# Kernel tuning notes

Measured on AMD Instinct MI355X. Metric: run time of the kernel, lower is better.

## Reference

```python
import jax, jax.numpy as jnp
import numpy as np

DIM = 1024

def setup_inputs() -> dict:
    key = jax.random.key(0)
    ks = jax.random.split(key, 7)
    s = 1.0 / np.sqrt(DIM)  # roughly match nn.Linear init scale
    return {
        "x": jax.random.normal(ks[0], (4, 2048, DIM), dtype=jnp.float32),
        "Wq": jax.random.normal(ks[1], (DIM, DIM), dtype=jnp.float32) * s,
        "bq": jax.random.normal(ks[2], (DIM,), dtype=jnp.float32) * s,
        "Wk": jax.random.normal(ks[3], (DIM, DIM), dtype=jnp.float32) * s,
        "bk": jax.random.normal(ks[4], (DIM,), dtype=jnp.float32) * s,
        "Wv": jax.random.normal(ks[5], (DIM, DIM), dtype=jnp.float32) * s,
        "bv": jax.random.normal(ks[6], (DIM,), dtype=jnp.float32) * s,
    }

def reference(x, Wq, bq, Wk, bk, Wv, bv):
    # torch Linear: y = x @ W.T + b
    C = x.shape[-1]
    scale = C ** (-0.5)
    q = jnp.einsum('bnc,dc->bnd', x, Wq) + bq
    k = jnp.einsum('bnc,dc->bnd', x, Wk) + bk
    v = jnp.einsum('bnc,dc->bnd', x, Wv) + bv
    attn = jnp.einsum('bnd,bmd->bnm', q, k) * scale  # [B,N,N]
    attn = jax.nn.softmax(attn, axis=-1)
    out = jnp.einsum('bnm,bmd->bnd', attn, v)
    return out
```

## Files before the change

kernel.cpp:

```cpp
#include <hip/hip_runtime.h>

#define SEQ  2048
#define DIM  1024
#define NTOK 8192
#define NQKV 3072

typedef __attribute__((ext_vector_type(8))) __bf16 bf16x8;
typedef __attribute__((ext_vector_type(4))) float  f32x4;

__device__ __forceinline__ unsigned short f2bf(float f) {
    unsigned int u = __float_as_uint(f);
    u += 0x7fffu + ((u >> 16) & 1u);
    return (unsigned short)(u >> 16);
}

__device__ __forceinline__ float bfu2f(unsigned int lo16) {
    return __uint_as_float(lo16 << 16);
}

__device__ __forceinline__ void load_lds_128(const unsigned short* g, unsigned short* l) {
    __builtin_amdgcn_global_load_lds(
        (const __attribute__((address_space(1))) void*)g,
        (__attribute__((address_space(3))) void*)l, 16, 0, 0);
}

#define BAR() asm volatile("s_barrier" ::: "memory")

template <int MODE, int MB>
__global__ __launch_bounds__(512, 2)
void gemm2(const unsigned short* __restrict__ A, const unsigned short* __restrict__ B,
           void* __restrict__ Cv,
           const float* __restrict__ b0v, const float* __restrict__ b1v,
           const float* __restrict__ b2v, unsigned short* __restrict__ vt,
           const float* __restrict__ inv_rs,
           int K, int lda, int ldb, int ldc,
           long sA, long sB, long sC, float alpha)
{
    constexpr int BM = MB * 128;
    constexpr int AT = BM * 64;
    constexpr int BT = 256 * 64;
    constexpr int MH = MB * 2;
    __shared__ __align__(16) unsigned short As[2 * AT];
    __shared__ __align__(16) unsigned short Bs[2 * BT];

    const int tid  = threadIdx.x;
    const int wave = tid >> 6;
    const int lane = tid & 63;
    const int l4   = lane & 15;
    const int lh   = lane >> 4;
    const int wm   = wave >> 2;
    const int wn   = wave & 3;

    const int m0 = blockIdx.x * BM;
    const int n0 = blockIdx.y * 256;
    const int z  = blockIdx.z;
    A += (long)z * sA;
    B += (long)z * sB;

    const int r0 = tid >> 3;
    const int gc = (tid & 7) ^ (r0 & 7);
    const unsigned short* Ag = A + (long)(m0 + r0) * lda + gc * 8;
    const unsigned short* Bg = B + (long)(n0 + r0) * ldb + gc * 8;
    unsigned short* Al = As + tid * 8;
    unsigned short* Bl = Bs + tid * 8;

    const int NT = K >> 6;

    auto stage = [&](int t, int u) {
        const long kof = (long)t * 64;
#pragma unroll
        for (int p = 0; p < 2 * MB; ++p)
            load_lds_128(Ag + kof + (long)(64 * p) * lda, Al + u * AT + p * 4096);
#pragma unroll
        for (int p = 0; p < 4; ++p)
            load_lds_128(Bg + kof + (long)(64 * p) * ldb, Bl + u * BT + p * 4096);
    };

    const int aoff = (wm * (BM / 2) + l4) * 64;
    const int boff = (wn * 64 + l4) * 64;
    const int cs0  = ((0 + lh) ^ (lane & 7)) * 8;
    const int cs1  = ((4 + lh) ^ (lane & 7)) * 8;

    f32x4 acc[4 * MB][4] = {};
    bf16x8 alo[MH][2], ahi[MH][2], bfr[4][2];

    stage(0, 0);
    asm volatile("s_waitcnt vmcnt(0)" ::: "memory");
    BAR();

    for (int t = 0; t < NT; ++t) {
        const int u = t & 1;
        const unsigned short* Ab = As + u * AT + aoff;
        const unsigned short* Bb = Bs + u * BT + boff;

        if (t + 1 < NT) stage(t + 1, u ^ 1);

#pragma unroll
        for (int nf = 0; nf < 4; ++nf) {
            bfr[nf][0] = *(const bf16x8*)(Bb + nf * 1024 + cs0);
            bfr[nf][1] = *(const bf16x8*)(Bb + nf * 1024 + cs1);
        }
#pragma unroll
        for (int mf = 0; mf < MH; ++mf) {
            alo[mf][0] = *(const bf16x8*)(Ab + mf * 1024 + cs0);
            alo[mf][1] = *(const bf16x8*)(Ab + mf * 1024 + cs1);
        }
#pragma unroll
        for (int mf = 0; mf < MH; ++mf) {
            ahi[mf][0] = *(const bf16x8*)(Ab + (MH + mf) * 1024 + cs0);
            ahi[mf][1] = *(const bf16x8*)(Ab + (MH + mf) * 1024 + cs1);
        }

        __builtin_amdgcn_s_setprio(1);
#pragma unroll
        for (int mf = 0; mf < MH; ++mf)
#pragma unroll
            for (int nf = 0; nf < 2; ++nf)
#pragma unroll
                for (int kk = 0; kk < 2; ++kk)
                    acc[mf][nf] = __builtin_amdgcn_mfma_f32_16x16x32_bf16(
                        alo[mf][kk], bfr[nf][kk], acc[mf][nf], 0, 0, 0);
        __builtin_amdgcn_s_setprio(0);
        __builtin_amdgcn_s_setprio(1);
#pragma unroll
        for (int mf = 0; mf < MH; ++mf)
#pragma unroll
            for (int nf = 2; nf < 4; ++nf)
#pragma unroll
                for (int kk = 0; kk < 2; ++kk)
                    acc[mf][nf] = __builtin_amdgcn_mfma_f32_16x16x32_bf16(
                        alo[mf][kk], bfr[nf][kk], acc[mf][nf], 0, 0, 0);
        __builtin_amdgcn_s_setprio(0);
        __builtin_amdgcn_s_setprio(1);
#pragma unroll
        for (int mf = 0; mf < MH; ++mf)
#pragma unroll
            for (int nf = 2; nf < 4; ++nf)
#pragma unroll
                for (int kk = 0; kk < 2; ++kk)
                    acc[MH + mf][nf] = __builtin_amdgcn_mfma_f32_16x16x32_bf16(
                        ahi[mf][kk], bfr[nf][kk], acc[MH + mf][nf], 0, 0, 0);
        __builtin_amdgcn_s_setprio(0);
        __builtin_amdgcn_s_setprio(1);
#pragma unroll
        for (int mf = 0; mf < MH; ++mf)
#pragma unroll
            for (int nf = 0; nf < 2; ++nf)
#pragma unroll
                for (int kk = 0; kk < 2; ++kk)
                    acc[MH + mf][nf] = __builtin_amdgcn_mfma_f32_16x16x32_bf16(
                        ahi[mf][kk], bfr[nf][kk], acc[MH + mf][nf], 0, 0, 0);
        __builtin_amdgcn_s_setprio(0);

        asm volatile("s_waitcnt vmcnt(0) lgkmcnt(0)" ::: "memory");
        BAR();
    }

    const int r0c = m0 + wm * (BM / 2) + lh * 4;
    const int c0c = n0 + wn * 64 + l4;

    if (MODE == 0) {
        if (n0 >= 2048) {
#pragma unroll
            for (int nf = 0; nf < 4; ++nf) {
                const int d = c0c + nf * 16 - 2048;
                const float bias = b2v[d];
#pragma unroll
                for (int mf = 0; mf < 4 * MB; ++mf) {
                    const int row = r0c + mf * 16;
                    const int bb = row >> 11;
                    const int mm = row & 2047;
                    ushort4 u;
                    u.x = f2bf(acc[mf][nf][0] + bias);
                    u.y = f2bf(acc[mf][nf][1] + bias);
                    u.z = f2bf(acc[mf][nf][2] + bias);
                    u.w = f2bf(acc[mf][nf][3] + bias);
                    *(ushort4*)(vt + ((long)bb * DIM + d) * SEQ + mm) = u;
                }
            }
        } else {
            unsigned short* C16 = (unsigned short*)Cv;
#pragma unroll
            for (int nf = 0; nf < 4; ++nf) {
                const int col = c0c + nf * 16;
                const float bias = (col >= 1024) ? b1v[col - 1024] : b0v[col];
#pragma unroll
                for (int mf = 0; mf < 4 * MB; ++mf)
#pragma unroll
                    for (int r = 0; r < 4; ++r)
                        C16[(long)(r0c + mf * 16 + r) * ldc + col] =
                            f2bf(acc[mf][nf][r] + bias);
            }
        }
    } else if (MODE == 1) {
        float* C = (float*)Cv + (long)z * sC;
        const float* ir = inv_rs + (long)z * SEQ;
#pragma unroll
        for (int mf = 0; mf < 4 * MB; ++mf) {
            const int row = r0c + mf * 16;
            const float4 inv4 = *(const float4*)(ir + row);
#pragma unroll
            for (int nf = 0; nf < 4; ++nf) {
                const int col = c0c + nf * 16;
                C[(long)(row + 0) * ldc + col] = acc[mf][nf][0] * inv4.x;
                C[(long)(row + 1) * ldc + col] = acc[mf][nf][1] * inv4.y;
                C[(long)(row + 2) * ldc + col] = acc[mf][nf][2] * inv4.z;
                C[(long)(row + 3) * ldc + col] = acc[mf][nf][3] * inv4.w;
            }
        }
    } else {
        unsigned short* C16 = (unsigned short*)Cv + (long)z * sC;
#pragma unroll
        for (int nf = 0; nf < 4; ++nf) {
            const int col = c0c + nf * 16;
#pragma unroll
            for (int mf = 0; mf < 4 * MB; ++mf)
#pragma unroll
                for (int r = 0; r < 4; ++r)
                    C16[(long)(r0c + mf * 16 + r) * ldc + col] =
                        f2bf(__expf(acc[mf][nf][r] * alpha));
        }
    }
}

__global__ __launch_bounds__(256)
void cvt_x(const float* __restrict__ src, unsigned short* __restrict__ dst, int n4)
{
    int i = blockIdx.x * 256 + threadIdx.x;
    if (i < n4) {
        float4 f = ((const float4*)src)[i];
        ushort4 u;
        u.x = f2bf(f.x); u.y = f2bf(f.y); u.z = f2bf(f.z); u.w = f2bf(f.w);
        ((ushort4*)dst)[i] = u;
    }
}

__global__ __launch_bounds__(256)
void cvt_w3(const float* __restrict__ Wq, const float* __restrict__ Wk,
            const float* __restrict__ Wv, unsigned short* __restrict__ dst)
{
    const int sel = blockIdx.y;
    const float* src = (sel == 0) ? Wq : ((sel == 1) ? Wk : Wv);
    const int i = blockIdx.x * 256 + threadIdx.x;
    float4 f = ((const float4*)src)[i];
    ushort4 u;
    u.x = f2bf(f.x); u.y = f2bf(f.y); u.z = f2bf(f.z); u.w = f2bf(f.w);
    ((ushort4*)(dst + (long)sel * DIM * DIM))[i] = u;
}

__global__ __launch_bounds__(256)
void rowsum_inv(const unsigned short* __restrict__ P, float* __restrict__ inv_rs)
{
    const int row  = blockIdx.x * 4 + (threadIdx.x >> 6);
    const int lane = threadIdx.x & 63;
    const unsigned short* pr = P + (long)row * SEQ;

    float s = 0.f;
#pragma unroll
    for (int it = 0; it < 4; ++it) {
        uint4 u = *(const uint4*)(pr + (it * 64 + lane) * 8);
        s += bfu2f(u.x & 0xffffu) + __uint_as_float(u.x & 0xffff0000u);
        s += bfu2f(u.y & 0xffffu) + __uint_as_float(u.y & 0xffff0000u);
        s += bfu2f(u.z & 0xffffu) + __uint_as_float(u.z & 0xffff0000u);
        s += bfu2f(u.w & 0xffffu) + __uint_as_float(u.w & 0xffff0000u);
    }
    for (int off = 32; off > 0; off >>= 1)
        s += __shfl_xor(s, off);
    if (lane == 0) inv_rs[row] = 1.0f / s;
}

extern "C" void kernel_launch(void* const* d_in, const int* in_sizes, int n_in,
                              void* d_out, int out_size, void* d_ws, size_t ws_size,
                              hipStream_t stream)
{
    const float* x  = (const float*)d_in[0];
    const float* Wq = (const float*)d_in[1];
    const float* bq = (const float*)d_in[2];
    const float* Wk = (const float*)d_in[3];
    const float* bk = (const float*)d_in[4];
    const float* Wv = (const float*)d_in[5];
    const float* bv = (const float*)d_in[6];
    float* out = (float*)d_out;

    char* ws = (char*)d_ws;
    unsigned short* xb   = (unsigned short*)ws;
    unsigned short* Wb   = (unsigned short*)(ws + 16u * 1024 * 1024);
    unsigned short* qkv  = (unsigned short*)(ws + 64u * 1024 * 1024);
    unsigned short* vt   = (unsigned short*)(ws + 112u * 1024 * 1024);
    unsigned short* P    = (unsigned short*)(ws + 128u * 1024 * 1024);
    float*          irs  = (float*)(ws + 160u * 1024 * 1024);

    const float scale = 0.03125f;
    dim3 blk(256);
    dim3 blk512(512);

    cvt_x<<<NTOK * DIM / 4 / 256, blk, 0, stream>>>(x, xb, NTOK * DIM / 4);
    cvt_w3<<<dim3(DIM * DIM / 4 / 256, 3), blk, 0, stream>>>(Wq, Wk, Wv, Wb);

    gemm2<0, 2><<<dim3(NTOK / 256, NQKV / 256), blk512, 0, stream>>>(
        xb, Wb, qkv, bq, bk, bv, vt, nullptr,
        DIM, DIM, DIM, NQKV, 0, 0, 0, 1.0f);

    gemm2<2, 2><<<dim3(SEQ / 256, SEQ / 256, 4), blk512, 0, stream>>>(
        qkv, qkv + 1024, P, nullptr, nullptr, nullptr, nullptr, nullptr,
        DIM, NQKV, NQKV, SEQ,
        (long)SEQ * NQKV, (long)SEQ * NQKV, (long)SEQ * SEQ, scale);

    rowsum_inv<<<NTOK / 4, blk, 0, stream>>>(P, irs);

    gemm2<1, 1><<<dim3(SEQ / 128, DIM / 256, 4), blk512, 0, stream>>>(
        P, vt, out, nullptr, nullptr, nullptr, nullptr, irs,
        SEQ, SEQ, SEQ, DIM,
        (long)SEQ * SEQ, (long)DIM * SEQ, (long)SEQ * DIM, 1.0f);
}
```

Measured before the change: 272.9 us.

## Overlap next-tile prefetch and barrier with MFMA clusters, shrink QKV GEMM tile

Restructures the GEMM main loop. All fragments are now read from LDS before the next-tile global→LDS stage is issued. The ahi fragment loads are interleaved between MFMA clusters. The wait/barrier moves ahead of the last MFMA cluster so synchronisation overlaps with compute. The QKV projection GEMM also switches from 256-row to 128-row tiles (MB=1), doubling its grid, to improve occupancy and wave balance. The added risk is the reordered wait and barrier: the final cluster runs after the barrier using register fragments, which is only safe if every LDS read has completed first.

```diff
diff --git a/kernel.cpp b/kernel.cpp
--- a/kernel.cpp
+++ b/kernel.cpp
@@ -25,6 +25,22 @@
 }
 
 #define BAR() asm volatile("s_barrier" ::: "memory")
+
+#define CLUSTER(AFR, NB, MBASE)                                            \
+    do {                                                                   \
+        __builtin_amdgcn_s_setprio(1);                                     \
+        _Pragma("unroll")                                                  \
+        for (int mf = 0; mf < 4; ++mf)                                     \
+            _Pragma("unroll")                                              \
+            for (int nn = 0; nn < 2; ++nn)                                 \
+                _Pragma("unroll")                                          \
+                for (int kk = 0; kk < 2; ++kk)                             \
+                    acc[(MBASE) + mf][(NB) + nn] =                         \
+                        __builtin_amdgcn_mfma_f32_16x16x32_bf16(           \
+                            AFR[mf][kk], bfr[(NB) + nn][kk],               \
+                            acc[(MBASE) + mf][(NB) + nn], 0, 0, 0);        \
+        __builtin_amdgcn_s_setprio(0);                                     \
+    } while (0)
 
 template <int MODE, int MB>
 __global__ __launch_bounds__(512, 2)
@@ -39,7 +55,6 @@
     constexpr int BM = MB * 128;
     constexpr int AT = BM * 64;
     constexpr int BT = 256 * 64;
-    constexpr int MH = MB * 2;
     __shared__ __align__(16) unsigned short As[2 * AT];
     __shared__ __align__(16) unsigned short Bs[2 * BT];
 
@@ -82,7 +97,7 @@
     const int cs1  = ((4 + lh) ^ (lane & 7)) * 8;
 
     f32x4 acc[4 * MB][4] = {};
-    bf16x8 alo[MH][2], ahi[MH][2], bfr[4][2];
+    bf16x8 bfr[4][2], alo[4][2], ahi[4][2];
 
     stage(0, 0);
     asm volatile("s_waitcnt vmcnt(0)" ::: "memory");
@@ -93,67 +108,41 @@
         const unsigned short* Ab = As + u * AT + aoff;
         const unsigned short* Bb = Bs + u * BT + boff;
 
-        if (t + 1 < NT) stage(t + 1, u ^ 1);
-
-#pragma unroll
-        for (int nf = 0; nf < 4; ++nf) {
-            bfr[nf][0] = *(const bf16x8*)(Bb + nf * 1024 + cs0);
-            bfr[nf][1] = *(const bf16x8*)(Bb + nf * 1024 + cs1);
-        }
-#pragma unroll
-        for (int mf = 0; mf < MH; ++mf) {
+#pragma unroll
+        for (int nn = 0; nn < 2; ++nn) {
+            bfr[nn][0] = *(const bf16x8*)(Bb + nn * 1024 + cs0);
+            bfr[nn][1] = *(const bf16x8*)(Bb + nn * 1024 + cs1);
+        }
+#pragma unroll
+        for (int mf = 0; mf < 4; ++mf) {
             alo[mf][0] = *(const bf16x8*)(Ab + mf * 1024 + cs0);
             alo[mf][1] = *(const bf16x8*)(Ab + mf * 1024 + cs1);
         }
 #pragma unroll
-        for (int mf = 0; mf < MH; ++mf) {
-            ahi[mf][0] = *(const bf16x8*)(Ab + (MH + mf) * 1024 + cs0);
-            ahi[mf][1] = *(const bf16x8*)(Ab + (MH + mf) * 1024 + cs1);
-        }
-
-        __builtin_amdgcn_s_setprio(1);
-#pragma unroll
-        for (int mf = 0; mf < MH; ++mf)
-#pragma unroll
-            for (int nf = 0; nf < 2; ++nf)
-#pragma unroll
-                for (int kk = 0; kk < 2; ++kk)
-                    acc[mf][nf] = __builtin_amdgcn_mfma_f32_16x16x32_bf16(
-                        alo[mf][kk], bfr[nf][kk], acc[mf][nf], 0, 0, 0);
-        __builtin_amdgcn_s_setprio(0);
-        __builtin_amdgcn_s_setprio(1);
-#pragma unroll
-        for (int mf = 0; mf < MH; ++mf)
-#pragma unroll
-            for (int nf = 2; nf < 4; ++nf)
-#pragma unroll
-                for (int kk = 0; kk < 2; ++kk)
-                    acc[mf][nf] = __builtin_amdgcn_mfma_f32_16x16x32_bf16(
-                        alo[mf][kk], bfr[nf][kk], acc[mf][nf], 0, 0, 0);
-        __builtin_amdgcn_s_setprio(0);
-        __builtin_amdgcn_s_setprio(1);
-#pragma unroll
-        for (int mf = 0; mf < MH; ++mf)
-#pragma unroll
-            for (int nf = 2; nf < 4; ++nf)
-#pragma unroll
-                for (int kk = 0; kk < 2; ++kk)
-                    acc[MH + mf][nf] = __builtin_amdgcn_mfma_f32_16x16x32_bf16(
-                        ahi[mf][kk], bfr[nf][kk], acc[MH + mf][nf], 0, 0, 0);
-        __builtin_amdgcn_s_setprio(0);
-        __builtin_amdgcn_s_setprio(1);
-#pragma unroll
-        for (int mf = 0; mf < MH; ++mf)
-#pragma unroll
-            for (int nf = 0; nf < 2; ++nf)
-#pragma unroll
-                for (int kk = 0; kk < 2; ++kk)
-                    acc[MH + mf][nf] = __builtin_amdgcn_mfma_f32_16x16x32_bf16(
-                        ahi[mf][kk], bfr[nf][kk], acc[MH + mf][nf], 0, 0, 0);
-        __builtin_amdgcn_s_setprio(0);
-
-        asm volatile("s_waitcnt vmcnt(0) lgkmcnt(0)" ::: "memory");
-        BAR();
+        for (int nn = 2; nn < 4; ++nn) {
+            bfr[nn][0] = *(const bf16x8*)(Bb + nn * 1024 + cs0);
+            bfr[nn][1] = *(const bf16x8*)(Bb + nn * 1024 + cs1);
+        }
+        if (t + 1 < NT) stage(t + 1, u ^ 1);
+
+        if constexpr (MB == 2) {
+            CLUSTER(alo, 0, 0);
+#pragma unroll
+            for (int mf = 0; mf < 4; ++mf) {
+                ahi[mf][0] = *(const bf16x8*)(Ab + (4 + mf) * 1024 + cs0);
+                ahi[mf][1] = *(const bf16x8*)(Ab + (4 + mf) * 1024 + cs1);
+            }
+            CLUSTER(alo, 2, 0);
+            CLUSTER(ahi, 2, 4);
+            asm volatile("s_waitcnt vmcnt(0) lgkmcnt(0)" ::: "memory");
+            BAR();
+            CLUSTER(ahi, 0, 4);
+        } else {
+            CLUSTER(alo, 0, 0);
+            asm volatile("s_waitcnt vmcnt(0) lgkmcnt(0)" ::: "memory");
+            BAR();
+            CLUSTER(alo, 2, 0);
+        }
     }
 
     const int r0c = m0 + wm * (BM / 2) + lh * 4;
@@ -297,7 +286,7 @@
     cvt_x<<<NTOK * DIM / 4 / 256, blk, 0, stream>>>(x, xb, NTOK * DIM / 4);
     cvt_w3<<<dim3(DIM * DIM / 4 / 256, 3), blk, 0, stream>>>(Wq, Wk, Wv, Wb);
 
-    gemm2<0, 2><<<dim3(NTOK / 256, NQKV / 256), blk512, 0, stream>>>(
+    gemm2<0, 1><<<dim3(NTOK / 128, NQKV / 256), blk512, 0, stream>>>(
         xb, Wb, qkv, bq, bk, bv, vt, nullptr,
         DIM, DIM, DIM, NQKV, 0, 0, 0, 1.0f);
 
```

Result: faster. 252.1 us (-7.6%).
